# Kernel tuning notes

Measured on AMD Instinct MI355X. Metric: run time of the kernel, lower is better.

Reference implementation:

```python
import jax, jax.numpy as jnp
import numpy as np
import math

BS, SEQ, D_IN, H, D_H = 2, 2048, 1024, 16, 64


def setup_inputs() -> dict:
    key = jax.random.key(0)
    ks = jax.random.split(key, 8)
    scale = 1.0 / math.sqrt(D_IN)
    inp = {
        "x": jax.random.normal(ks[0], (BS, SEQ, D_IN), dtype=jnp.float32),
        "attention_mask": jnp.zeros((BS, SEQ), dtype=jnp.float32),
        # Linear params: torch nn.Linear stores weight [out, in]; we keep [in, out].
        "Wq": jax.random.normal(ks[1], (D_IN, H * D_H), dtype=jnp.float32) * scale,
        "bq": jnp.zeros((H * D_H,), dtype=jnp.float32),
        "Wk": jax.random.normal(ks[2], (D_IN, H * D_H), dtype=jnp.float32) * scale,
        "bk": jnp.zeros((H * D_H,), dtype=jnp.float32),
        "Wv": jax.random.normal(ks[3], (D_IN, H * D_H), dtype=jnp.float32) * scale,
        "bv": jnp.zeros((H * D_H,), dtype=jnp.float32),
    }
    return inp


def reference(x, attention_mask, Wq, bq, Wk, bk, Wv, bv):
    bs, seq_len, _ = x.shape
    # QKV projections -> [b, h, s, d]
    def proj(W, b):
        return (x @ W + b).reshape(bs, seq_len, H, D_H).transpose(0, 2, 1, 3)

    q = proj(Wq, bq) * (1.0 / math.sqrt(D_H))
    k = proj(Wk, bk)
    v = proj(Wv, bv)

    # scores [b, h, s_q, s_k]
    scores = jnp.einsum("bhid,bhjd->bhij", q, k)
    scores = scores + attention_mask[:, None, None, :]
    attn = jax.nn.softmax(scores, axis=-1)
    ctx = jnp.einsum("bhij,bhjd->bhid", attn, v)
    # [b, s, h*d]
    return ctx.transpose(0, 2, 1, 3).reshape(bs, seq_len, H * D_H)
```

## Files before the change

### kernel.cpp

```cpp
#include <hip/hip_runtime.h>
#include <hip/hip_bf16.h>

#define BSZ 2
#define SEQ 2048
#define DIN 1024
#define NH 16
#define DH 64
#define NTOK (BSZ*SEQ)
#define NQ (NH*DH)

typedef __bf16 bf16x8 __attribute__((ext_vector_type(8)));
typedef float f32x4 __attribute__((ext_vector_type(4)));

#define LOG2E 1.4426950408889634f
#define QSCALE (0.125f * LOG2E)

__device__ __forceinline__ void gl_lds16(const void* g, void* l) {
  __builtin_amdgcn_global_load_lds(
      (__attribute__((address_space(1))) void*)(g),
      (__attribute__((address_space(3))) void*)(l), 16, 0, 0);
}

__device__ __forceinline__ bf16x8 ld16(const void* p) {
  union { uint4 u; bf16x8 b; } t;
  t.u = *(const uint4*)p;
  return t.b;
}

__device__ __forceinline__ unsigned short bfbits(float f) {
  union { __bf16 h; unsigned short u; } c; c.h = (__bf16)f; return c.u;
}

__global__ __launch_bounds__(256) void pack_x_k(const float* __restrict__ x,
                                                __bf16* __restrict__ xb) {
  int i = blockIdx.x * 256 + threadIdx.x;
  const float4* p = (const float4*)x + (size_t)2 * i;
  float4 a = p[0], b = p[1];
  union { unsigned short s[8]; uint4 u; } o;
  o.s[0] = bfbits(a.x); o.s[1] = bfbits(a.y); o.s[2] = bfbits(a.z); o.s[3] = bfbits(a.w);
  o.s[4] = bfbits(b.x); o.s[5] = bfbits(b.y); o.s[6] = bfbits(b.z); o.s[7] = bfbits(b.w);
  ((uint4*)xb)[i] = o.u;
}

__global__ __launch_bounds__(256) void pack_w_k(const float* __restrict__ Wq,
                                                const float* __restrict__ Wk,
                                                const float* __restrict__ Wv,
                                                __bf16* __restrict__ Wt) {
  __shared__ float t[32][33];
  int mz = blockIdx.z;
  const float* W = (mz == 0) ? Wq : ((mz == 1) ? Wk : Wv);
  int k0 = blockIdx.x * 32, n0 = blockIdx.y * 32;
  int tx = threadIdx.x & 31, ty = threadIdx.x >> 5;
  #pragma unroll
  for (int i = 0; i < 4; i++)
    t[ty + 8 * i][tx] = W[(size_t)(k0 + ty + 8 * i) * NQ + n0 + tx];
  __syncthreads();
  #pragma unroll
  for (int i = 0; i < 4; i++)
    Wt[(size_t)(mz * NQ + n0 + ty + 8 * i) * DIN + k0 + tx] = (__bf16)t[tx][ty + 8 * i];
}

__global__ __launch_bounds__(256, 2) void qkv_gemm_k(
    const __bf16* __restrict__ Wt, const __bf16* __restrict__ Xb,
    const float* __restrict__ bq, const float* __restrict__ bk2,
    const float* __restrict__ bv,
    __bf16* __restrict__ Qs, __bf16* __restrict__ Kg, __bf16* __restrict__ Vt) {
  __shared__ unsigned char Asm[128 * 128];
  __shared__ unsigned char Bsm[128 * 128];
  const int tid = threadIdx.x;
  const int lane = tid & 63, wave = tid >> 6;
  const int nb = blockIdx.x * 128, mb = blockIdx.y * 128;
  const int wn = (wave >> 1) * 64, wm = (wave & 1) * 64;
  f32x4 acc[4][4] = {};

  for (int kk = 0; kk < DIN; kk += 64) {
    #pragma unroll
    for (int i = 0; i < 4; i++) {
      int o = (i * 256 + tid) * 16;
      int row = o >> 7;
      int sch = ((o >> 4) & 7) ^ (row & 7);
      gl_lds16((const char*)Wt + (size_t)(nb + row) * 2048 + kk * 2 + sch * 16,
               Asm + (i * 4 + wave) * 1024);
      gl_lds16((const char*)Xb + (size_t)(mb + row) * 2048 + kk * 2 + sch * 16,
               Bsm + (i * 4 + wave) * 1024);
    }
    __syncthreads();
    #pragma unroll
    for (int kt = 0; kt < 2; kt++) {
      bf16x8 af[4], bfr[4];
      #pragma unroll
      for (int mt = 0; mt < 4; mt++) {
        int row = wn + mt * 16 + (lane & 15);
        int byo = (row * 128 + (kt * 32 + (lane >> 4) * 8) * 2) ^ ((row & 7) << 4);
        af[mt] = ld16(Asm + byo);
      }
      #pragma unroll
      for (int nt = 0; nt < 4; nt++) {
        int row = wm + nt * 16 + (lane & 15);
        int byo = (row * 128 + (kt * 32 + (lane >> 4) * 8) * 2) ^ ((row & 7) << 4);
        bfr[nt] = ld16(Bsm + byo);
      }
      #pragma unroll
      for (int mt = 0; mt < 4; mt++)
        #pragma unroll
        for (int nt = 0; nt < 4; nt++)
          acc[mt][nt] = __builtin_amdgcn_mfma_f32_16x16x32_bf16(af[mt], bfr[nt], acc[mt][nt], 0, 0, 0);
    }
    __syncthreads();
  }

  #pragma unroll
  for (int mt = 0; mt < 4; mt++) {
    int n0 = nb + wn + mt * 16 + ((lane >> 4) << 2);
    int mat = n0 >> 10;
    int c0 = n0 & 1023;
    int h = c0 >> 6, d0 = c0 & 63;
    #pragma unroll
    for (int nt = 0; nt < 4; nt++) {
      int m = mb + wm + nt * 16 + (lane & 15);
      int b = m >> 11, s = m & 2047;
      f32x4 v = acc[mt][nt];
      if (mat == 0) {
        ushort4 pk;
        pk.x = bfbits((v[0] + bq[c0 + 0]) * QSCALE);
        pk.y = bfbits((v[1] + bq[c0 + 1]) * QSCALE);
        pk.z = bfbits((v[2] + bq[c0 + 2]) * QSCALE);
        pk.w = bfbits((v[3] + bq[c0 + 3]) * QSCALE);
        *(ushort4*)(Qs + ((size_t)((b * NH + h) * SEQ + s)) * DH + d0) = pk;
      } else if (mat == 1) {
        ushort4 pk;
        pk.x = bfbits(v[0] + bk2[c0 + 0]);
        pk.y = bfbits(v[1] + bk2[c0 + 1]);
        pk.z = bfbits(v[2] + bk2[c0 + 2]);
        pk.w = bfbits(v[3] + bk2[c0 + 3]);
        *(ushort4*)(Kg + ((size_t)((b * NH + h) * SEQ + s)) * DH + d0) = pk;
      } else {
        #pragma unroll
        for (int r = 0; r < 4; r++)
          Vt[((size_t)((b * NH + h) * DH + d0 + r)) * SEQ + s] = (__bf16)(v[r] + bv[c0 + r]);
      }
    }
  }
}

__global__ __launch_bounds__(256, 4) void attn_k(
    const __bf16* __restrict__ Qs, const __bf16* __restrict__ Kg,
    const __bf16* __restrict__ Vt, const float* __restrict__ mask,
    float* __restrict__ out) {
  __shared__ unsigned char Ksm[2][64 * 128];
  __shared__ unsigned char Vsm[2][64 * 128];
  __shared__ unsigned char Psm[4][16 * 128];
  const int tid = threadIdx.x, lane = tid & 63, wave = tid >> 6;
  const int bh = blockIdx.y, b = bh >> 4, h = bh & 15;
  const int qw = blockIdx.x * 64 + wave * 16;
  const __bf16* Qh = Qs + (size_t)bh * SEQ * DH;
  const char* Kh = (const char*)(Kg + (size_t)bh * SEQ * DH);
  const char* Vh = (const char*)(Vt + (size_t)bh * DH * SEQ);
  const float* mbase = mask + b * SEQ;

  bf16x8 qf[2];
  #pragma unroll
  for (int kt = 0; kt < 2; kt++)
    qf[kt] = ld16(Qh + (size_t)(qw + (lane & 15)) * DH + kt * 32 + (lane >> 4) * 8);

  f32x4 oacc[4] = {};
  float mcur = -1e30f, lrow = 0.f;

  const int g16 = (lane >> 4) * 16;

  #define STAGE(buf, kv)                                                        \
    {                                                                           \
      _Pragma("unroll")                                                         \
      for (int i = 0; i < 2; i++) {                                             \
        int o = (i * 256 + tid) * 16;                                           \
        int row = o >> 7;                                                       \
        int sch = ((o >> 4) & 7) ^ (row & 7);                                   \
        gl_lds16(Kh + (size_t)((kv) + row) * 128 + sch * 16,                    \
                 Ksm[buf] + (i * 4 + wave) * 1024);                             \
        gl_lds16(Vh + (size_t)row * (SEQ * 2) + (kv) * 2 + sch * 16,            \
                 Vsm[buf] + (i * 4 + wave) * 1024);                             \
      }                                                                         \
    }

  STAGE(0, 0);
  __syncthreads();
  int cur = 0;

  for (int t = 0; t < SEQ / 64; t++) {
    const int kv = t * 64;
    if (t + 1 < SEQ / 64) STAGE(cur ^ 1, kv + 64);

    f32x4 sacc[4] = {};
    #pragma unroll
    for (int kt = 0; kt < 2; kt++) {
      #pragma unroll
      for (int nt = 0; nt < 4; nt++) {
        int row = nt * 16 + (lane & 15);
        int byo = (row * 128 + kt * 64 + g16) ^ ((row & 7) << 4);
        bf16x8 kf = ld16(Ksm[cur] + byo);
        sacc[nt] = __builtin_amdgcn_mfma_f32_16x16x32_bf16(kf, qf[kt], sacc[nt], 0, 0, 0);
      }
    }

    #pragma unroll
    for (int nt = 0; nt < 4; nt++) {
      f32x4 mq = *(const f32x4*)(mbase + kv + nt * 16 + ((lane >> 4) << 2));
      #pragma unroll
      for (int r = 0; r < 4; r++) sacc[nt][r] += mq[r] * LOG2E;
    }

    float px = sacc[0][0];
    #pragma unroll
    for (int nt = 0; nt < 4; nt++)
      #pragma unroll
      for (int r = 0; r < 4; r++) px = fmaxf(px, sacc[nt][r]);
    px = fmaxf(px, __shfl_xor(px, 16));
    px = fmaxf(px, __shfl_xor(px, 32));

    if (__any(px > mcur + 8.0f)) {
      float mnew = fmaxf(mcur, px);
      float al = __builtin_exp2f(mcur - mnew);
      mcur = mnew;
      lrow *= al;
      #pragma unroll
      for (int r = 0; r < 4; r++) {
        float alr = __shfl(al, ((lane >> 4) << 2) + r);
        #pragma unroll
        for (int nt = 0; nt < 4; nt++) oacc[nt][r] *= alr;
      }
    }

    float ps = 0.f;
    #pragma unroll
    for (int nt = 0; nt < 4; nt++)
      #pragma unroll
      for (int r = 0; r < 4; r++) {
        float p = __builtin_exp2f(sacc[nt][r] - mcur);
        sacc[nt][r] = p;
        ps += p;
      }
    ps += __shfl_xor(ps, 16);
    ps += __shfl_xor(ps, 32);
    lrow += ps;

    #pragma unroll
    for (int nt = 0; nt < 4; nt++) {
      ushort4 pk;
      pk.x = bfbits(sacc[nt][0]); pk.y = bfbits(sacc[nt][1]);
      pk.z = bfbits(sacc[nt][2]); pk.w = bfbits(sacc[nt][3]);
      int byo = ((lane & 15) * 128 + nt * 32 + (lane >> 4) * 8) ^ ((lane & 7) << 4);
      *(ushort4*)(Psm[wave] + byo) = pk;
    }

    #pragma unroll
    for (int kt = 0; kt < 2; kt++) {
      int pbyo = ((lane & 15) * 128 + kt * 64 + g16) ^ ((lane & 7) << 4);
      bf16x8 pf = ld16(Psm[wave] + pbyo);
      #pragma unroll
      for (int nt = 0; nt < 4; nt++) {
        int vrow = nt * 16 + (lane & 15);
        int vbyo = (vrow * 128 + kt * 64 + g16) ^ ((vrow & 7) << 4);
        bf16x8 vf = ld16(Vsm[cur] + vbyo);
        oacc[nt] = __builtin_amdgcn_mfma_f32_16x16x32_bf16(pf, vf, oacc[nt], 0, 0, 0);
      }
    }
    __syncthreads();
    cur ^= 1;
  }

  float linv = 1.0f / lrow;
  #pragma unroll
  for (int r = 0; r < 4; r++) {
    float li = __shfl(linv, ((lane >> 4) << 2) + r);
    int s = qw + ((lane >> 4) << 2) + r;
    #pragma unroll
    for (int nt = 0; nt < 4; nt++) {
      int d = nt * 16 + (lane & 15);
      out[(size_t)(b * SEQ + s) * NQ + h * DH + d] = oacc[nt][r] * li;
    }
  }
}

extern "C" void kernel_launch(void* const* d_in, const int* in_sizes, int n_in,
                              void* d_out, int out_size, void* d_ws, size_t ws_size,
                              hipStream_t stream) {
  (void)in_sizes; (void)n_in; (void)out_size; (void)ws_size;
  const float* x   = (const float*)d_in[0];
  const float* msk = (const float*)d_in[1];
  const float* Wq  = (const float*)d_in[2];
  const float* bq  = (const float*)d_in[3];
  const float* Wk  = (const float*)d_in[4];
  const float* bk  = (const float*)d_in[5];
  const float* Wv  = (const float*)d_in[6];
  const float* bv  = (const float*)d_in[7];
  float* out = (float*)d_out;

  char* ws = (char*)d_ws;
  __bf16* Xb = (__bf16*)(ws);
  __bf16* Wt = (__bf16*)(ws + ((size_t)8 << 20));
  __bf16* Qs = (__bf16*)(ws + ((size_t)14 << 20));
  __bf16* Kg = (__bf16*)(ws + ((size_t)22 << 20));
  __bf16* Vt = (__bf16*)(ws + ((size_t)30 << 20));

  pack_x_k<<<2048, 256, 0, stream>>>(x, Xb);
  pack_w_k<<<dim3(32, 32, 3), 256, 0, stream>>>(Wq, Wk, Wv, Wt);
  qkv_gemm_k<<<dim3(24, 32), 256, 0, stream>>>(Wt, Xb, bq, bk, bv, Qs, Kg, Vt);
  attn_k<<<dim3(32, 32), 256, 0, stream>>>(Qs, Kg, Vt, msk, out);
}
```

Measured before the change: 200.6 us.

## Swizzle block order, precompute mask, MFMA row sums, unroll attention loop

Remaps block IDs in the QKV GEMM and attention kernels so that concurrently running blocks are spread across XCDs and reuse K/V in cache. A small kernel pre-scales the mask by log2(e), and the attention scores accumulator is initialized from that mask instead of having it added afterward. Row sums of P are now computed with an extra MFMA against a ones vector in place of shuffle reductions. The KV loop is unrolled by two with static buffer indices, LDS offsets are precomputed, and s_setprio wraps the MFMA sections. These add one kernel launch and one extra MFMA per k-step. Row sums now come from bf16-rounded P, which slightly changes numerics.

Result: faster. 194.7 us (-2.9%).

```diff
diff --git a/kernel.cpp b/kernel.cpp
--- a/kernel.cpp
+++ b/kernel.cpp
@@ -42,6 +42,12 @@
   ((uint4*)xb)[i] = o.u;
 }
 
+__global__ __launch_bounds__(256) void pack_m_k(const float* __restrict__ m,
+                                                float* __restrict__ m2) {
+  int i = blockIdx.x * 256 + threadIdx.x;
+  m2[i] = m[i] * LOG2E;
+}
+
 __global__ __launch_bounds__(256) void pack_w_k(const float* __restrict__ Wq,
                                                 const float* __restrict__ Wk,
                                                 const float* __restrict__ Wv,
@@ -69,7 +75,9 @@
   __shared__ unsigned char Bsm[128 * 128];
   const int tid = threadIdx.x;
   const int lane = tid & 63, wave = tid >> 6;
-  const int nb = blockIdx.x * 128, mb = blockIdx.y * 128;
+  const int lid = blockIdx.y * 24 + blockIdx.x;
+  const int swz = (lid & 7) * 96 + (lid >> 3);
+  const int nb = (swz % 24) * 128, mb = (swz / 24) * 128;
   const int wn = (wave >> 1) * 64, wm = (wave & 1) * 64;
   f32x4 acc[4][4] = {};
 
@@ -145,18 +153,20 @@
 
 __global__ __launch_bounds__(256, 4) void attn_k(
     const __bf16* __restrict__ Qs, const __bf16* __restrict__ Kg,
-    const __bf16* __restrict__ Vt, const float* __restrict__ mask,
+    const __bf16* __restrict__ Vt, const float* __restrict__ m2,
     float* __restrict__ out) {
   __shared__ unsigned char Ksm[2][64 * 128];
   __shared__ unsigned char Vsm[2][64 * 128];
   __shared__ unsigned char Psm[4][16 * 128];
   const int tid = threadIdx.x, lane = tid & 63, wave = tid >> 6;
-  const int bh = blockIdx.y, b = bh >> 4, h = bh & 15;
-  const int qw = blockIdx.x * 64 + wave * 16;
+  const int id = blockIdx.y * 32 + blockIdx.x;
+  const int sid = (id & 7) * 128 + (id >> 3);
+  const int bh = sid >> 5, b = bh >> 4, h = bh & 15;
+  const int qw = (sid & 31) * 64 + wave * 16;
   const __bf16* Qh = Qs + (size_t)bh * SEQ * DH;
   const char* Kh = (const char*)(Kg + (size_t)bh * SEQ * DH);
   const char* Vh = (const char*)(Vt + (size_t)bh * DH * SEQ);
-  const float* mbase = mask + b * SEQ;
+  const float* mb2 = m2 + b * SEQ;
 
   bf16x8 qf[2];
   #pragma unroll
@@ -164,9 +174,30 @@
     qf[kt] = ld16(Qh + (size_t)(qw + (lane & 15)) * DH + kt * 32 + (lane >> 4) * 8);
 
   f32x4 oacc[4] = {};
-  float mcur = -1e30f, lrow = 0.f;
+  f32x4 osum = {};
+  float mcur = -1e30f;
 
   const int g16 = (lane >> 4) * 16;
+
+  int fo[2][4];
+  #pragma unroll
+  for (int kt = 0; kt < 2; kt++)
+    #pragma unroll
+    for (int nt = 0; nt < 4; nt++) {
+      int row = nt * 16 + (lane & 15);
+      fo[kt][nt] = (row * 128 + kt * 64 + g16) ^ ((row & 7) << 4);
+    }
+  int prd[2], pwr[4];
+  #pragma unroll
+  for (int kt = 0; kt < 2; kt++)
+    prd[kt] = ((lane & 15) * 128 + kt * 64 + g16) ^ ((lane & 7) << 4);
+  #pragma unroll
+  for (int nt = 0; nt < 4; nt++)
+    pwr[nt] = ((lane & 15) * 128 + nt * 32 + (lane >> 4) * 8) ^ ((lane & 7) << 4);
+
+  bf16x8 ones;
+  #pragma unroll
+  for (int j = 0; j < 8; j++) ones[j] = (__bf16)1.0f;
 
   #define STAGE(buf, kv)                                                        \
     {                                                                           \
@@ -182,96 +213,81 @@
       }                                                                         \
     }
 
+  #define BODY(BUF, tt)                                                         \
+    {                                                                           \
+      const int kv = (tt) * 64;                                                 \
+      if ((tt) + 1 < 32) STAGE(BUF ^ 1, kv + 64);                               \
+      f32x4 sacc[4];                                                            \
+      _Pragma("unroll")                                                         \
+      for (int nt = 0; nt < 4; nt++)                                            \
+        sacc[nt] = *(const f32x4*)(mb2 + kv + nt * 16 + ((lane >> 4) << 2));    \
+      __builtin_amdgcn_s_setprio(1);                                            \
+      _Pragma("unroll")                                                         \
+      for (int kt = 0; kt < 2; kt++) {                                          \
+        _Pragma("unroll")                                                       \
+        for (int nt = 0; nt < 4; nt++) {                                        \
+          bf16x8 kf = ld16(Ksm[BUF] + fo[kt][nt]);                              \
+          sacc[nt] = __builtin_amdgcn_mfma_f32_16x16x32_bf16(kf, qf[kt], sacc[nt], 0, 0, 0); \
+        }                                                                       \
+      }                                                                         \
+      __builtin_amdgcn_s_setprio(0);                                            \
+      float px = sacc[0][0];                                                    \
+      _Pragma("unroll")                                                         \
+      for (int nt = 0; nt < 4; nt++)                                            \
+        _Pragma("unroll")                                                       \
+        for (int r = 0; r < 4; r++) px = fmaxf(px, sacc[nt][r]);                \
+      px = fmaxf(px, __shfl_xor(px, 16));                                       \
+      px = fmaxf(px, __shfl_xor(px, 32));                                       \
+      if (__any(px > mcur + 8.0f)) {                                            \
+        float mnew = fmaxf(mcur, px);                                           \
+        float al = __builtin_exp2f(mcur - mnew);                                \
+        mcur = mnew;                                                            \
+        _Pragma("unroll")                                                       \
+        for (int r = 0; r < 4; r++) {                                           \
+          float alr = __shfl(al, ((lane >> 4) << 2) + r);                       \
+          _Pragma("unroll")                                                     \
+          for (int nt = 0; nt < 4; nt++) oacc[nt][r] *= alr;                    \
+          osum[r] *= alr;                                                       \
+        }                                                                       \
+      }                                                                         \
+      _Pragma("unroll")                                                         \
+      for (int nt = 0; nt < 4; nt++)                                            \
+        _Pragma("unroll")                                                       \
+        for (int r = 0; r < 4; r++)                                             \
+          sacc[nt][r] = __builtin_exp2f(sacc[nt][r] - mcur);                    \
+      _Pragma("unroll")                                                         \
+      for (int nt = 0; nt < 4; nt++) {                                          \
+        ushort4 pk;                                                             \
+        pk.x = bfbits(sacc[nt][0]); pk.y = bfbits(sacc[nt][1]);                 \
+        pk.z = bfbits(sacc[nt][2]); pk.w = bfbits(sacc[nt][3]);                 \
+        *(ushort4*)(Psm[wave] + pwr[nt]) = pk;                                  \
+      }                                                                         \
+      __builtin_amdgcn_s_setprio(1);                                            \
+      _Pragma("unroll")                                                         \
+      for (int kt = 0; kt < 2; kt++) {                                          \
+        bf16x8 pf = ld16(Psm[wave] + prd[kt]);                                  \
+        osum = __builtin_amdgcn_mfma_f32_16x16x32_bf16(pf, ones, osum, 0, 0, 0); \
+        _Pragma("unroll")                                                       \
+        for (int nt = 0; nt < 4; nt++) {                                        \
+          bf16x8 vf = ld16(Vsm[BUF] + fo[kt][nt]);                              \
+          oacc[nt] = __builtin_amdgcn_mfma_f32_16x16x32_bf16(pf, vf, oacc[nt], 0, 0, 0); \
+        }                                                                       \
+      }                                                                         \
+      __builtin_amdgcn_s_setprio(0);                                            \
+      __syncthreads();                                                          \
+    }
+
   STAGE(0, 0);
   __syncthreads();
-  int cur = 0;
-
-  for (int t = 0; t < SEQ / 64; t++) {
-    const int kv = t * 64;
-    if (t + 1 < SEQ / 64) STAGE(cur ^ 1, kv + 64);
-
-    f32x4 sacc[4] = {};
-    #pragma unroll
-    for (int kt = 0; kt < 2; kt++) {
-      #pragma unroll
-      for (int nt = 0; nt < 4; nt++) {
-        int row = nt * 16 + (lane & 15);
-        int byo = (row * 128 + kt * 64 + g16) ^ ((row & 7) << 4);
-        bf16x8 kf = ld16(Ksm[cur] + byo);
-        sacc[nt] = __builtin_amdgcn_mfma_f32_16x16x32_bf16(kf, qf[kt], sacc[nt], 0, 0, 0);
-      }
-    }
-
-    #pragma unroll
-    for (int nt = 0; nt < 4; nt++) {
-      f32x4 mq = *(const f32x4*)(mbase + kv + nt * 16 + ((lane >> 4) << 2));
-      #pragma unroll
-      for (int r = 0; r < 4; r++) sacc[nt][r] += mq[r] * LOG2E;
-    }
-
-    float px = sacc[0][0];
-    #pragma unroll
-    for (int nt = 0; nt < 4; nt++)
-      #pragma unroll
-      for (int r = 0; r < 4; r++) px = fmaxf(px, sacc[nt][r]);
-    px = fmaxf(px, __shfl_xor(px, 16));
-    px = fmaxf(px, __shfl_xor(px, 32));
-
-    if (__any(px > mcur + 8.0f)) {
-      float mnew = fmaxf(mcur, px);
-      float al = __builtin_exp2f(mcur - mnew);
-      mcur = mnew;
-      lrow *= al;
-      #pragma unroll
-      for (int r = 0; r < 4; r++) {
-        float alr = __shfl(al, ((lane >> 4) << 2) + r);
-        #pragma unroll
-        for (int nt = 0; nt < 4; nt++) oacc[nt][r] *= alr;
-      }
-    }
-
-    float ps = 0.f;
-    #pragma unroll
-    for (int nt = 0; nt < 4; nt++)
-      #pragma unroll
-      for (int r = 0; r < 4; r++) {
-        float p = __builtin_exp2f(sacc[nt][r] - mcur);
-        sacc[nt][r] = p;
-        ps += p;
-      }
-    ps += __shfl_xor(ps, 16);
-    ps += __shfl_xor(ps, 32);
-    lrow += ps;
-
-    #pragma unroll
-    for (int nt = 0; nt < 4; nt++) {
-      ushort4 pk;
-      pk.x = bfbits(sacc[nt][0]); pk.y = bfbits(sacc[nt][1]);
-      pk.z = bfbits(sacc[nt][2]); pk.w = bfbits(sacc[nt][3]);
-      int byo = ((lane & 15) * 128 + nt * 32 + (lane >> 4) * 8) ^ ((lane & 7) << 4);
-      *(ushort4*)(Psm[wave] + byo) = pk;
-    }
-
-    #pragma unroll
-    for (int kt = 0; kt < 2; kt++) {
-      int pbyo = ((lane & 15) * 128 + kt * 64 + g16) ^ ((lane & 7) << 4);
-      bf16x8 pf = ld16(Psm[wave] + pbyo);
-      #pragma unroll
-      for (int nt = 0; nt < 4; nt++) {
-        int vrow = nt * 16 + (lane & 15);
-        int vbyo = (vrow * 128 + kt * 64 + g16) ^ ((vrow & 7) << 4);
-        bf16x8 vf = ld16(Vsm[cur] + vbyo);
-        oacc[nt] = __builtin_amdgcn_mfma_f32_16x16x32_bf16(pf, vf, oacc[nt], 0, 0, 0);
-      }
-    }
-    __syncthreads();
-    cur ^= 1;
+
+  for (int t = 0; t < 32; t += 2) {
+    BODY(0, t)
+    BODY(1, t + 1)
   }
 
-  float linv = 1.0f / lrow;
   #pragma unroll
   for (int r = 0; r < 4; r++) {
-    float li = __shfl(linv, ((lane >> 4) << 2) + r);
+    float li = 1.0f / osum[r];
     int s = qw + ((lane >> 4) << 2) + r;
     #pragma unroll
     for (int nt = 0; nt < 4; nt++) {
@@ -279,6 +295,8 @@
       out[(size_t)(b * SEQ + s) * NQ + h * DH + d] = oacc[nt][r] * li;
     }
   }
+  #undef BODY
+  #undef STAGE
 }
 
 extern "C" void kernel_launch(void* const* d_in, const int* in_sizes, int n_in,
@@ -301,9 +319,11 @@
   __bf16* Qs = (__bf16*)(ws + ((size_t)14 << 20));
   __bf16* Kg = (__bf16*)(ws + ((size_t)22 << 20));
   __bf16* Vt = (__bf16*)(ws + ((size_t)30 << 20));
+  float*  m2 = (float*) (ws + ((size_t)38 << 20));
 
   pack_x_k<<<2048, 256, 0, stream>>>(x, Xb);
+  pack_m_k<<<16, 256, 0, stream>>>(msk, m2);
   pack_w_k<<<dim3(32, 32, 3), 256, 0, stream>>>(Wq, Wk, Wv, Wt);
   qkv_gemm_k<<<dim3(24, 32), 256, 0, stream>>>(Wt, Xb, bq, bk, bv, Qs, Kg, Vt);
-  attn_k<<<dim3(32, 32), 256, 0, stream>>>(Qs, Kg, Vt, msk, out);
-}
+  attn_k<<<dim3(32, 32), 256, 0, stream>>>(Qs, Kg, Vt, m2, out);
+}
```
